# Kernel tuning notes

Hardware: AMD Instinct MI355X
Metric: run time of the kernel (lower is better)

Reference implementation:

```python
import jax, jax.numpy as jnp
import numpy as np
import math

D_MODEL = 128      # embedding_dim
D_STATE = 64
D_CONV = 4
NHEADS = 4         # d_inner / headdim (Mamba2 default headdim=64)
HEADDIM = 64
D_INNER = 256      # expand * d_model
CONV_DIM = 384     # d_inner + 2*ngroups*d_state (ngroups=1)
D_IN_PROJ = 644    # 2*d_inner + 2*ngroups*d_state + nheads
NLAYERS = 2
INPUT_DIM = 768
EPS = 1e-5


def setup_inputs() -> dict:
    key = jax.random.key(0)
    ks = jax.random.split(key, 20)
    rn = lambda k, s, sd=0.02: jax.random.normal(k, s, jnp.float32) * sd
    return {
        "x": jax.random.normal(ks[0], (16, 1024, INPUT_DIM), jnp.float32),
        "fc1_W": rn(ks[1], (INPUT_DIM, D_MODEL)),
        "fc1_b": jnp.zeros((D_MODEL,), jnp.float32),
        "ln_w": jnp.ones((NLAYERS, D_MODEL), jnp.float32),
        "ln_b": jnp.zeros((NLAYERS, D_MODEL), jnp.float32),
        "in_W": rn(ks[2], (NLAYERS, D_MODEL, D_IN_PROJ)),
        "conv_w": rn(ks[3], (NLAYERS, D_CONV, CONV_DIM), 0.1),
        "conv_b": jnp.zeros((NLAYERS, CONV_DIM), jnp.float32),
        "dt_bias": rn(ks[4], (NLAYERS, NHEADS), 0.5),
        "A_log": jnp.log(jax.random.uniform(ks[5], (NLAYERS, NHEADS), jnp.float32, 1.0, 16.0)),
        "Dp": jnp.ones((NLAYERS, NHEADS), jnp.float32),
        "rms_w": jnp.ones((NLAYERS, D_INNER), jnp.float32),
        "out_W": rn(ks[6], (NLAYERS, D_INNER, D_MODEL)),
        "fc2_W1": rn(ks[7], (D_MODEL, D_MODEL)),
        "fc2_b1": jnp.zeros((D_MODEL,), jnp.float32),
        "fc2_W2": rn(ks[8], (D_MODEL, 6)),
        "fc2_b2": jnp.zeros((6,), jnp.float32),
    }


def _pos_embedding(L):
    pos = jnp.arange(L, dtype=jnp.float32)[:, None]                       # (L,1)
    div = jnp.exp(jnp.arange(0, D_MODEL, 2, dtype=jnp.float32) * (-math.log(10000.0) / D_MODEL))
    pe = jnp.zeros((L, D_MODEL), jnp.float32)
    pe = pe.at[:, 0::2].set(jnp.sin(pos * div))
    pe = pe.at[:, 1::2].set(jnp.cos(pos * div))
    return pe[None]                                                        # (1,L,D)


def _layernorm(x, w, b):
    mu = jnp.mean(x, -1, keepdims=True)
    var = jnp.mean(jnp.square(x - mu), -1, keepdims=True)
    return (x - mu) * jax.lax.rsqrt(var + EPS) * w + b


def _mamba2(u, in_W, conv_w, conv_b, dt_bias, A_log, Dp, rms_w, out_W):
    b, l, _ = u.shape
    zxbcdt = u @ in_W                                                      # (b,l,644)
    z = zxbcdt[..., :D_INNER]
    xBC = zxbcdt[..., D_INNER:D_INNER + CONV_DIM]
    dt = jax.nn.softplus(zxbcdt[..., D_INNER + CONV_DIM:] + dt_bias)       # (b,l,h)
    # causal depthwise conv1d (width 4) + SiLU
    xp = jnp.pad(xBC, ((0, 0), (D_CONV - 1, 0), (0, 0)))
    xc = conv_b
    for k in range(D_CONV):
        xc = xc + conv_w[k] * xp[:, k:k + l, :]
    xc = jax.nn.silu(xc)                                                   # (b,l,384)
    xh = xc[..., :D_INNER].reshape(b, l, NHEADS, HEADDIM)                  # (b,l,h,p)
    B = xc[..., D_INNER:D_INNER + D_STATE]                                 # (b,l,n)
    C = xc[..., D_INNER + D_STATE:]                                        # (b,l,n)
    A = -jnp.exp(A_log)                                                    # (h,)
    dA = jnp.exp(dt * A)                                                   # (b,l,h)
    dtx = dt[..., None] * xh                                               # (b,l,h,p)

    def step(h, inp):
        dA_t, dtx_t, B_t, C_t = inp                                        # (b,h),(b,h,p),(b,n),(b,n)
        h = dA_t[..., None, None] * h + dtx_t[..., None] * B_t[:, None, None, :]
        y = jnp.einsum('bhpn,bn->bhp', h, C_t)
        return h, y

    h0 = jnp.zeros((b, NHEADS, HEADDIM, D_STATE), u.dtype)
    _, ys = jax.lax.scan(step, h0, (dA.transpose(1, 0, 2), dtx.transpose(1, 0, 2, 3),
                                    B.transpose(1, 0, 2), C.transpose(1, 0, 2)))
    y = ys.transpose(1, 0, 2, 3) + Dp[None, None, :, None] * xh            # (b,l,h,p)
    y = y.reshape(b, l, D_INNER)
    # gated RMSNorm: rmsnorm(y * silu(z)) * weight
    y = y * jax.nn.silu(z)
    y = y * jax.lax.rsqrt(jnp.mean(jnp.square(y), -1, keepdims=True) + EPS) * rms_w
    return y @ out_W


def reference(x, fc1_W, fc1_b, ln_w, ln_b, in_W, conv_w, conv_b, dt_bias,
              A_log, Dp, rms_w, out_W, fc2_W1, fc2_b1, fc2_W2, fc2_b2):
    h = x @ fc1_W + fc1_b                                                  # (b,l,128)
    h = h + _pos_embedding(h.shape[1])
    for i in range(NLAYERS):
        res = h
        hn = _layernorm(h, ln_w[i], ln_b[i])
        h = _mamba2(hn, in_W[i], conv_w[i], conv_b[i], dt_bias[i],
                    A_log[i], Dp[i], rms_w[i], out_W[i]) + res
        # dropout: identity in eval mode
    h = jax.nn.leaky_relu(h @ fc2_W1 + fc2_b1, negative_slope=0.1)
    return h @ fc2_W2 + fc2_b2                                             # (b,l,6)
```

## Files before the change

### kernel.cpp

```cpp
#include <hip/hip_runtime.h>
#include <hip/hip_bf16.h>

#define BATCH 16
#define SEQ 1024
#define NROWS (BATCH*SEQ)
#define IN_DIM 768
#define DM 128
#define DIP 644
#define DI 256
#define CDIM 384
#define DST 64
#define NH 4
#define HD 64
#define CHUNK 64
#define NCHUNK (SEQ/CHUNK)

#define WB_FC1   0
#define WB_IN    98304
#define WB_OUT   263168
#define WB_FC2   328704
#define WB_TOTAL 345088

typedef __attribute__((ext_vector_type(8))) short short8;
typedef __attribute__((ext_vector_type(4))) float float4v;

__device__ __forceinline__ short f2b(float f) {
    unsigned u = __builtin_bit_cast(unsigned, f);
    u += 0x7fffu + ((u >> 16) & 1u);
    return (short)(u >> 16);
}
__device__ __forceinline__ short8 pack8f(float4 a, float4 b) {
    short8 r;
    r[0] = f2b(a.x); r[1] = f2b(a.y); r[2] = f2b(a.z); r[3] = f2b(a.w);
    r[4] = f2b(b.x); r[5] = f2b(b.y); r[6] = f2b(b.z); r[7] = f2b(b.w);
    return r;
}

__global__ void prep_weights(const float* __restrict__ fc1_W, const float* __restrict__ in_W,
                             const float* __restrict__ out_W, const float* __restrict__ fc2_W1,
                             short* __restrict__ wb) {
    int idx = blockIdx.x * 256 + threadIdx.x;
    if (idx < 98304) {
        int n = idx / 768, k = idx % 768;
        wb[WB_FC1 + idx] = f2b(fc1_W[k * 128 + n]);
        return;
    }
    idx -= 98304;
    if (idx < 2 * 82432) {
        int l = idx / 82432, r = idx % 82432;
        int n = r / 128, k = r % 128;
        wb[WB_IN + idx] = f2b(in_W[(size_t)l * 82432 + k * 644 + n]);
        return;
    }
    idx -= 164864;
    if (idx < 2 * 32768) {
        int l = idx / 32768, r = idx % 32768;
        int n = r / 256, k = r % 256;
        wb[WB_OUT + idx] = f2b(out_W[(size_t)l * 32768 + k * 128 + n]);
        return;
    }
    idx -= 65536;
    if (idx < 16384) {
        int n = idx / 128, k = idx % 128;
        wb[WB_FC2 + idx] = f2b(fc2_W1[k * 128 + n]);
    }
}

#define GEMM_PROLOGUE() \
    int tid = threadIdx.x; \
    int lane = tid & 63; \
    int m = lane & 15; \
    int kq = (lane >> 4) * 8; \
    int w = tid >> 6; \
    int mrow = (w & 3) * 16; \
    int ngrp = w >> 2; \
    int a_off = (mrow + m) * 72 + kq; \
    int b_off = (ngrp * 64 + m) * 72 + kq; \
    int ar = tid >> 3; \
    int ak = (tid & 7) * 8; \
    (void)ar; (void)ak; \
    float4v acc[4]; \
    acc[0] = (float4v)0.f; acc[1] = (float4v)0.f; acc[2] = (float4v)0.f; acc[3] = (float4v)0.f;

#define GEMM_COMPUTE_TILE() \
    { \
        short8 a0 = *reinterpret_cast<const short8*>(&As[a_off]); \
        short8 a1 = *reinterpret_cast<const short8*>(&As[a_off + 32]); \
        _Pragma("unroll") \
        for (int nt = 0; nt < 4; nt++) { \
            short8 b0 = *reinterpret_cast<const short8*>(&Bt[b_off + nt * 16 * 72]); \
            short8 b1 = *reinterpret_cast<const short8*>(&Bt[b_off + nt * 16 * 72 + 32]); \
            acc[nt] = __builtin_amdgcn_mfma_f32_16x16x32_bf16(a0, b0, acc[nt], 0, 0, 0); \
            acc[nt] = __builtin_amdgcn_mfma_f32_16x16x32_bf16(a1, b1, acc[nt], 0, 0, 0); \
        } \
    }

#define GEMM_STAGE_B(wtptr, LDB, k0) \
    _Pragma("unroll") \
    for (int i = 0; i < 2; i++) { \
        int idx = tid + i * 512; \
        int n = idx >> 3, kk = (idx & 7) * 8; \
        *reinterpret_cast<short8*>(&Bt[n * 72 + kk]) = \
            *reinterpret_cast<const short8*>(&wtptr[n * (LDB) + (k0) + kk]); \
    }

__global__ __launch_bounds__(512) void fc1_mfma(const float* __restrict__ x,
                                                const short* __restrict__ wt,
                                                const float* __restrict__ bias,
                                                float* __restrict__ h) {
    __shared__ short As[64 * 72];
    __shared__ short Bt[128 * 72];
    GEMM_PROLOGUE();
    int row0 = blockIdx.x * 64;
    for (int kt = 0; kt < 12; kt++) {
        int k0 = kt * 64;
        if (kt) __syncthreads();
        {
            const float* src = x + (size_t)(row0 + ar) * IN_DIM + k0 + ak;
            float4 v0 = *(const float4*)src;
            float4 v1 = *(const float4*)(src + 4);
            *reinterpret_cast<short8*>(&As[ar * 72 + ak]) = pack8f(v0, v1);
        }
        GEMM_STAGE_B(wt, 768, k0);
        __syncthreads();
        GEMM_COMPUTE_TILE();
    }
    #pragma unroll
    for (int nt = 0; nt < 4; nt++) {
        int col = ngrp * 64 + nt * 16 + m;
        float bv = bias[col];
        float div = expf(-(float)(col & ~1) * 0.071955784f);
        #pragma unroll
        for (int r = 0; r < 4; r++) {
            int row = row0 + mrow + (lane >> 4) * 4 + r;
            int t = row & (SEQ - 1);
            float arg = (float)t * div;
            float pe = (col & 1) ? cosf(arg) : sinf(arg);
            h[(size_t)row * DM + col] = acc[nt][r] + bv + pe;
        }
    }
}

__global__ __launch_bounds__(512) void inproj_ln_mfma(const float* __restrict__ h,
                                                      const float* __restrict__ lnw,
                                                      const float* __restrict__ lnb,
                                                      const short* __restrict__ wb,
                                                      float* __restrict__ zx, int layer) {
    __shared__ short As[64 * 72];
    __shared__ short Bt[128 * 72];
    __shared__ float mu_s[64], rs_s[64];
    GEMM_PROLOGUE();
    int row0 = blockIdx.x * 64;
    int ncol0 = blockIdx.y * 128;
    const short* wt = wb + WB_IN + (size_t)layer * 82432;
    {
        int r = tid >> 3, j = tid & 7;
        const float4* hr = (const float4*)(h + (size_t)(row0 + r) * DM + j * 16);
        float s1 = 0.f, s2 = 0.f;
        #pragma unroll
        for (int i = 0; i < 4; i++) {
            float4 v = hr[i];
            s1 += v.x + v.y + v.z + v.w;
            s2 += v.x * v.x + v.y * v.y + v.z * v.z + v.w * v.w;
        }
        #pragma unroll
        for (int o = 1; o < 8; o <<= 1) { s1 += __shfl_xor(s1, o); s2 += __shfl_xor(s2, o); }
        if (j == 0) {
            float mu = s1 * (1.f / 128.f);
            mu_s[r] = mu;
            rs_s[r] = rsqrtf(s2 * (1.f / 128.f) - mu * mu + 1e-5f);
        }
    }
    __syncthreads();
    for (int kt = 0; kt < 2; kt++) {
        int k0 = kt * 64;
        if (kt) __syncthreads();
        {
            int k = k0 + ak;
            const float* src = h + (size_t)(row0 + ar) * DM + k;
            float4 v0 = *(const float4*)src;
            float4 v1 = *(const float4*)(src + 4);
            float4 w0 = *(const float4*)(lnw + layer * DM + k);
            float4 w1 = *(const float4*)(lnw + layer * DM + k + 4);
            float4 b0 = *(const float4*)(lnb + layer * DM + k);
            float4 b1 = *(const float4*)(lnb + layer * DM + k + 4);
            float mu = mu_s[ar], rs = rs_s[ar];
            v0.x = (v0.x - mu) * rs * w0.x + b0.x; v0.y = (v0.y - mu) * rs * w0.y + b0.y;
            v0.z = (v0.z - mu) * rs * w0.z + b0.z; v0.w = (v0.w - mu) * rs * w0.w + b0.w;
            v1.x = (v1.x - mu) * rs * w1.x + b1.x; v1.y = (v1.y - mu) * rs * w1.y + b1.y;
            v1.z = (v1.z - mu) * rs * w1.z + b1.z; v1.w = (v1.w - mu) * rs * w1.w + b1.w;
            *reinterpret_cast<short8*>(&As[ar * 72 + ak]) = pack8f(v0, v1);
        }
        #pragma unroll
        for (int i = 0; i < 2; i++) {
            int idx = tid + i * 512;
            int n = idx >> 3, kk = (idx & 7) * 8;
            int col = ncol0 + n;
            short8 bv = (short8)0;
            if (col < DIP) bv = *reinterpret_cast<const short8*>(&wt[col * 128 + k0 + kk]);
            *reinterpret_cast<short8*>(&Bt[n * 72 + kk]) = bv;
        }
        __syncthreads();
        GEMM_COMPUTE_TILE();
    }
    #pragma unroll
    for (int nt = 0; nt < 4; nt++) {
        int col = ncol0 + ngrp * 64 + nt * 16 + m;
        if (col < DIP) {
            #pragma unroll
            for (int r = 0; r < 4; r++) {
                int row = row0 + mrow + (lane >> 4) * 4 + r;
                zx[(size_t)row * DIP + col] = acc[nt][r];
            }
        }
    }
}

__global__ void conv_kernel(const float* __restrict__ zx, const float* __restrict__ convw,
                            const float* __restrict__ convb, const float* __restrict__ dt_bias,
                            float* __restrict__ xc, float* __restrict__ dtb, int layer) {
    int c = threadIdx.x;
    int row0 = blockIdx.x * 4;
    int l0 = row0 & (SEQ - 1);
    const float* cw = convw + (size_t)layer * 4 * CDIM;
    float w0 = cw[c], w1 = cw[CDIM + c], w2 = cw[2 * CDIM + c], w3 = cw[3 * CDIM + c];
    float bb = convb[layer * CDIM + c];
    float v[7];
    #pragma unroll
    for (int i = 0; i < 7; i++) {
        int rr = row0 + i - 3;
        v[i] = (l0 + i - 3 >= 0) ? zx[(size_t)rr * DIP + DI + c] : 0.f;
    }
    #pragma unroll
    for (int j = 0; j < 4; j++) {
        float acc = bb + w0 * v[j] + w1 * v[j + 1] + w2 * v[j + 2] + w3 * v[j + 3];
        float sv = acc / (1.f + expf(-acc));
        xc[(size_t)(row0 + j) * CDIM + c] = sv;
    }
    if (c < 16) {
        int j = c >> 2, hh = c & 3;
        int row = row0 + j;
        float raw = zx[(size_t)row * DIP + DI + CDIM + hh] + dt_bias[layer * NH + hh];
        float dt = (raw > 20.f) ? raw : log1pf(expf(raw));
        dtb[row * NH + hh] = dt;
    }
}

__global__ __launch_bounds__(256) void chunk_state_mfma(const float* __restrict__ xc,
                                                        const float* __restrict__ dtb,
                                                        const float* __restrict__ A_log,
                                                        float* __restrict__ Sloc,
                                                        float* __restrict__ decay, int layer) {
    __shared__ short XTw[64 * 72];
    __shared__ short BT[64 * 72];
    __shared__ float wst[64];
    int bid = blockIdx.x;
    int c  = bid & (NCHUNK - 1);
    int hh = (bid >> 4) & (NH - 1);
    int b  = bid >> 6;
    int tid = threadIdx.x;
    int row0 = b * SEQ + c * CHUNK;
    float A = -expf(A_log[layer * NH + hh]);

    if (tid < CHUNK) {
        float dtv = dtb[(row0 + tid) * NH + hh];
        float l = dtv * A;
        #pragma unroll
        for (int o = 1; o < 64; o <<= 1) { float v = __shfl_up(l, o); if (tid >= o) l += v; }
        float Ltot = __shfl(l, 63);
        wst[tid] = expf(Ltot - l) * dtv;
        if (tid == 63) decay[bid] = expf(Ltot);
    }
    __syncthreads();
    {
        int p = tid & 63;
        int tb0 = tid >> 6;
        #pragma unroll
        for (int i = 0; i < 2; i++) {
            int t0 = (tb0 + i * 4) * 8;
            short8 xv, bv;
            #pragma unroll
            for (int j = 0; j < 8; j++) {
                int t = t0 + j;
                const float* xr = xc + (size_t)(row0 + t) * CDIM;
                xv[j] = f2b(xr[hh * HD + p] * wst[t]);
                bv[j] = f2b(xr[DI + p]);
            }
            *reinterpret_cast<short8*>(&XTw[p * 72 + t0]) = xv;
            *reinterpret_cast<short8*>(&BT[p * 72 + t0]) = bv;
        }
    }
    __syncthreads();

    int lane = tid & 63;
    int m = lane & 15;
    int kq = (lane >> 4) * 8;
    int w = tid >> 6;
    int a_off = (w * 16 + m) * 72 + kq;
    float4v acc[4];
    acc[0] = (float4v)0.f; acc[1] = (float4v)0.f; acc[2] = (float4v)0.f; acc[3] = (float4v)0.f;
    short8 a0 = *reinterpret_cast<const short8*>(&XTw[a_off]);
    short8 a1 = *reinterpret_cast<const short8*>(&XTw[a_off + 32]);
    #pragma unroll
    for (int nt = 0; nt < 4; nt++) {
        int bo = (nt * 16 + m) * 72 + kq;
        short8 b0 = *reinterpret_cast<const short8*>(&BT[bo]);
        short8 b1 = *reinterpret_cast<const short8*>(&BT[bo + 32]);
        acc[nt] = __builtin_amdgcn_mfma_f32_16x16x32_bf16(a0, b0, acc[nt], 0, 0, 0);
        acc[nt] = __builtin_amdgcn_mfma_f32_16x16x32_bf16(a1, b1, acc[nt], 0, 0, 0);
    }
    float* Sp = Sloc + (size_t)bid * (HD * DST);
    int tq = (lane >> 4) * 4;
    #pragma unroll
    for (int nt = 0; nt < 4; nt++) {
        #pragma unroll
        for (int r = 0; r < 4; r++) {
            int p = w * 16 + tq + r;
            int n = nt * 16 + m;
            Sp[p * DST + n] = acc[nt][r];
        }
    }
}

__global__ void chunk_scan_kernel(const float* __restrict__ Sloc, const float* __restrict__ decay,
                                  float* __restrict__ hstart) {
    int bh = blockIdx.x;
    int tid = threadIdx.x;
    float hreg[16];
    #pragma unroll
    for (int k = 0; k < 16; k++) hreg[k] = 0.f;
    for (int c = 0; c < NCHUNK; c++) {
        size_t base = ((size_t)bh * NCHUNK + c) * (HD * DST);
        float d = decay[bh * NCHUNK + c];
        #pragma unroll
        for (int k = 0; k < 16; k++) {
            int i = tid + k * 256;
            hstart[base + i] = hreg[k];
            hreg[k] = d * hreg[k] + Sloc[base + i];
        }
    }
}

__global__ __launch_bounds__(256) void chunk_out_mfma(const float* __restrict__ xc,
                                                      const float* __restrict__ dtb,
                                                      const float* __restrict__ A_log,
                                                      const float* __restrict__ Dpw,
                                                      const float* __restrict__ hstart,
                                                      float* __restrict__ y, int layer) {
    __shared__ short Cb[64 * 72];
    __shared__ short Bb[64 * 72];
    __shared__ short XT[64 * 72];
    __shared__ short HT[64 * 72];
    __shared__ float Ls[64], dts[64];
    int bid = blockIdx.x;
    int c  = bid & (NCHUNK - 1);
    int hh = (bid >> 4) & (NH - 1);
    int b  = bid >> 6;
    int tid = threadIdx.x;
    int row0 = b * SEQ + c * CHUNK;
    float A = -expf(A_log[layer * NH + hh]);
    float Dph = Dpw[layer * NH + hh];

    if (tid < CHUNK) {
        float dtv = dtb[(row0 + tid) * NH + hh];
        float l = dtv * A;
        #pragma unroll
        for (int o = 1; o < 64; o <<= 1) { float v = __shfl_up(l, o); if (tid >= o) l += v; }
        Ls[tid] = l;
        dts[tid] = dtv;
    }
    {
        int p = tid & 63;
        int tb0 = tid >> 6;
        #pragma unroll
        for (int i = 0; i < 2; i++) {
            int t0 = (tb0 + i * 4) * 8;
            short8 xv;
            #pragma unroll
            for (int j = 0; j < 8; j++) {
                const float* xr = xc + (size_t)(row0 + t0 + j) * CDIM;
                xv[j] = f2b(xr[hh * HD + p]);
            }
            *reinterpret_cast<short8*>(&XT[p * 72 + t0]) = xv;
        }
    }
    #pragma unroll
    for (int i = 0; i < 2; i++) {
        int idx = tid + i * 256;
        int t = idx >> 3, cb = (idx & 7) * 8;
        const float* xr = xc + (size_t)(row0 + t) * CDIM;
        float4 b0 = *(const float4*)(xr + DI + cb);
        float4 b1 = *(const float4*)(xr + DI + cb + 4);
        *reinterpret_cast<short8*>(&Bb[t * 72 + cb]) = pack8f(b0, b1);
        float4 c0 = *(const float4*)(xr + DI + DST + cb);
        float4 c1 = *(const float4*)(xr + DI + DST + cb + 4);
        *reinterpret_cast<short8*>(&Cb[t * 72 + cb]) = pack8f(c0, c1);
    }
    {
        const float* hs = hstart + (size_t)bid * (HD * DST);
        #pragma unroll
        for (int i = 0; i < 2; i++) {
            int idx = tid + i * 256;
            int pp = idx >> 3, nb = (idx & 7) * 8;
            float4 a0 = *(const float4*)(hs + pp * 64 + nb);
            float4 a1 = *(const float4*)(hs + pp * 64 + nb + 4);
            *reinterpret_cast<short8*>(&HT[pp * 72 + nb]) = pack8f(a0, a1);
        }
    }
    __syncthreads();

    int lane = tid & 63;
    int m = lane & 15;
    int kq = (lane >> 4) * 8;
    int w = tid >> 6;
    int tq = (lane >> 4) * 4;
    int a_off = (w * 16 + m) * 72 + kq;

    short8 ca0 = *reinterpret_cast<const short8*>(&Cb[a_off]);
    short8 ca1 = *reinterpret_cast<const short8*>(&Cb[a_off + 32]);

    float4v g[4], ir[4];
    #pragma unroll
    for (int i = 0; i < 4; i++) { g[i] = (float4v)0.f; ir[i] = (float4v)0.f; }
    #pragma unroll
    for (int st = 0; st < 4; st++) {
        int bo = (st * 16 + m) * 72 + kq;
        short8 b0 = *reinterpret_cast<const short8*>(&Bb[bo]);
        short8 b1 = *reinterpret_cast<const short8*>(&Bb[bo + 32]);
        g[st] = __builtin_amdgcn_mfma_f32_16x16x32_bf16(ca0, b0, g[st], 0, 0, 0);
        g[st] = __builtin_amdgcn_mfma_f32_16x16x32_bf16(ca1, b1, g[st], 0, 0, 0);
        short8 h0 = *reinterpret_cast<const short8*>(&HT[bo]);
        short8 h1 = *reinterpret_cast<const short8*>(&HT[bo + 32]);
        ir[st] = __builtin_amdgcn_mfma_f32_16x16x32_bf16(ca0, h0, ir[st], 0, 0, 0);
        ir[st] = __builtin_amdgcn_mfma_f32_16x16x32_bf16(ca1, h1, ir[st], 0, 0, 0);
    }
    __syncthreads();
    #pragma unroll
    for (int st = 0; st < 4; st++) {
        #pragma unroll
        for (int r = 0; r < 4; r++) {
            int t = w * 16 + tq + r;
            int s = st * 16 + m;
            float mv = 0.f;
            if (s <= t) mv = g[st][r] * expf(Ls[t] - Ls[s]) * dts[s];
            Bb[t * 72 + s] = f2b(mv);
        }
    }
    __syncthreads();
    float4v yi[4];
    #pragma unroll
    for (int i = 0; i < 4; i++) yi[i] = (float4v)0.f;
    short8 ma0 = *reinterpret_cast<const short8*>(&Bb[a_off]);
    short8 ma1 = *reinterpret_cast<const short8*>(&Bb[a_off + 32]);
    #pragma unroll
    for (int pt = 0; pt < 4; pt++) {
        int bo = (pt * 16 + m) * 72 + kq;
        short8 x0 = *reinterpret_cast<const short8*>(&XT[bo]);
        short8 x1 = *reinterpret_cast<const short8*>(&XT[bo + 32]);
        yi[pt] = __builtin_amdgcn_mfma_f32_16x16x32_bf16(ma0, x0, yi[pt], 0, 0, 0);
        yi[pt] = __builtin_amdgcn_mfma_f32_16x16x32_bf16(ma1, x1, yi[pt], 0, 0, 0);
    }
    #pragma unroll
    for (int r = 0; r < 4; r++) {
        int t = w * 16 + tq + r;
        float et = expf(Ls[t]);
        const float* xr = xc + (size_t)(row0 + t) * CDIM + hh * HD;
        float* yr = y + (size_t)(row0 + t) * DI + hh * HD;
        #pragma unroll
        for (int pt = 0; pt < 4; pt++) {
            int p = pt * 16 + m;
            yr[p] = yi[pt][r] + et * ir[pt][r] + Dph * xr[p];
        }
    }
}

__global__ __launch_bounds__(512) void outproj_gate_mfma(const float* __restrict__ yb,
                                                         const float* __restrict__ zx,
                                                         const float* __restrict__ rmsw,
                                                         const short* __restrict__ wb,
                                                         float* __restrict__ h, int layer) {
    __shared__ short As[64 * 72];
    __shared__ short Bt[128 * 72];
    __shared__ float rs_s[64];
    GEMM_PROLOGUE();
    int row0 = blockIdx.x * 64;
    const short* wt = wb + WB_OUT + (size_t)layer * 32768;
    {
        int r = tid >> 3, j = tid & 7;
        const float4* yr = (const float4*)(yb + (size_t)(row0 + r) * DI + j * 32);
        const float4* zr = (const float4*)(zx + (size_t)(row0 + r) * DIP + j * 32);
        float s2 = 0.f;
        #pragma unroll
        for (int i = 0; i < 8; i++) {
            float4 yv = yr[i], zv = zr[i];
            float v;
            v = yv.x * (zv.x / (1.f + expf(-zv.x))); s2 += v * v;
            v = yv.y * (zv.y / (1.f + expf(-zv.y))); s2 += v * v;
            v = yv.z * (zv.z / (1.f + expf(-zv.z))); s2 += v * v;
            v = yv.w * (zv.w / (1.f + expf(-zv.w))); s2 += v * v;
        }
        #pragma unroll
        for (int o = 1; o < 8; o <<= 1) s2 += __shfl_xor(s2, o);
        if (j == 0) rs_s[r] = rsqrtf(s2 * (1.f / 256.f) + 1e-5f);
    }
    __syncthreads();
    for (int kt = 0; kt < 4; kt++) {
        int k0 = kt * 64;
        if (kt) __syncthreads();
        {
            int k = k0 + ak;
            const float* ysrc = yb + (size_t)(row0 + ar) * DI + k;
            const float* zsrc = zx + (size_t)(row0 + ar) * DIP + k;
            float4 y0 = *(const float4*)ysrc;
            float4 y1 = *(const float4*)(ysrc + 4);
            float4 z0 = *(const float4*)zsrc;
            float4 z1 = *(const float4*)(zsrc + 4);
            float4 w0 = *(const float4*)(rmsw + layer * DI + k);
            float4 w1 = *(const float4*)(rmsw + layer * DI + k + 4);
            float rs = rs_s[ar];
            y0.x = y0.x * (z0.x / (1.f + expf(-z0.x))) * rs * w0.x;
            y0.y = y0.y * (z0.y / (1.f + expf(-z0.y))) * rs * w0.y;
            y0.z = y0.z * (z0.z / (1.f + expf(-z0.z))) * rs * w0.z;
            y0.w = y0.w * (z0.w / (1.f + expf(-z0.w))) * rs * w0.w;
            y1.x = y1.x * (z1.x / (1.f + expf(-z1.x))) * rs * w1.x;
            y1.y = y1.y * (z1.y / (1.f + expf(-z1.y))) * rs * w1.y;
            y1.z = y1.z * (z1.z / (1.f + expf(-z1.z))) * rs * w1.z;
            y1.w = y1.w * (z1.w / (1.f + expf(-z1.w))) * rs * w1.w;
            *reinterpret_cast<short8*>(&As[ar * 72 + ak]) = pack8f(y0, y1);
        }
        GEMM_STAGE_B(wt, 256, k0);
        __syncthreads();
        GEMM_COMPUTE_TILE();
    }
    #pragma unroll
    for (int nt = 0; nt < 4; nt++) {
        int col = ngrp * 64 + nt * 16 + m;
        #pragma unroll
        for (int r = 0; r < 4; r++) {
            int row = row0 + mrow + (lane >> 4) * 4 + r;
            size_t i = (size_t)row * DM + col;
            h[i] = h[i] + acc[nt][r];
        }
    }
}

__global__ __launch_bounds__(512) void fc2ab_mfma(const float* __restrict__ h,
                                                  const short* __restrict__ wb,
                                                  const float* __restrict__ b1,
                                                  const float* __restrict__ W2,
                                                  const float* __restrict__ b2,
                                                  float* __restrict__ out) {
    __shared__ short As[64 * 72];
    __shared__ short Bt[128 * 72];
    __shared__ float h2s[64][132];
    __shared__ float w2s[768];
    GEMM_PROLOGUE();
    int row0 = blockIdx.x * 64;
    const short* wt = wb + WB_FC2;
    for (int i = tid; i < 768; i += 512) w2s[i] = W2[i];
    for (int kt = 0; kt < 2; kt++) {
        int k0 = kt * 64;
        if (kt) __syncthreads();
        {
            const float* src = h + (size_t)(row0 + ar) * DM + k0 + ak;
            float4 v0 = *(const float4*)src;
            float4 v1 = *(const float4*)(src + 4);
            *reinterpret_cast<short8*>(&As[ar * 72 + ak]) = pack8f(v0, v1);
        }
        GEMM_STAGE_B(wt, 128, k0);
        __syncthreads();
        GEMM_COMPUTE_TILE();
    }
    #pragma unroll
    for (int nt = 0; nt < 4; nt++) {
        int col = ngrp * 64 + nt * 16 + m;
        float bv = b1[col];
        #pragma unroll
        for (int r = 0; r < 4; r++) {
            int rr = mrow + (lane >> 4) * 4 + r;
            float o = acc[nt][r] + bv;
            h2s[rr][col] = (o > 0.f) ? o : 0.1f * o;
        }
    }
    __syncthreads();
    if (tid < 384) {
        int r = tid / 6, cc = tid % 6;
        float acc2 = b2[cc];
        #pragma unroll 16
        for (int k = 0; k < 128; k++) acc2 += h2s[r][k] * w2s[k * 6 + cc];
        out[(size_t)(row0 + r) * 6 + cc] = acc2;
    }
}

extern "C" void kernel_launch(void* const* d_in, const int* in_sizes, int n_in,
                              void* d_out, int out_size, void* d_ws, size_t ws_size,
                              hipStream_t stream) {
    const float* x       = (const float*)d_in[0];
    const float* fc1_W   = (const float*)d_in[1];
    const float* fc1_b   = (const float*)d_in[2];
    const float* ln_w    = (const float*)d_in[3];
    const float* ln_b    = (const float*)d_in[4];
    const float* in_W    = (const float*)d_in[5];
    const float* conv_w  = (const float*)d_in[6];
    const float* conv_b  = (const float*)d_in[7];
    const float* dt_bias = (const float*)d_in[8];
    const float* A_log   = (const float*)d_in[9];
    const float* Dp      = (const float*)d_in[10];
    const float* rms_w   = (const float*)d_in[11];
    const float* out_W   = (const float*)d_in[12];
    const float* fc2_W1  = (const float*)d_in[13];
    const float* fc2_b1  = (const float*)d_in[14];
    const float* fc2_W2  = (const float*)d_in[15];
    const float* fc2_b2  = (const float*)d_in[16];
    float* out = (float*)d_out;

    float* ws = (float*)d_ws;
    float* h     = ws;
    float* zx    = h     + (size_t)NROWS * DM;
    float* xc    = zx    + (size_t)NROWS * DIP;
    float* dtb   = xc    + (size_t)NROWS * CDIM;
    float* yb    = dtb   + (size_t)NROWS * NH;
    float* Sloc  = yb    + (size_t)NROWS * DI;
    float* hstr  = Sloc  + (size_t)BATCH*NH*NCHUNK*HD*DST;
    float* decay = hstr  + (size_t)BATCH*NH*NCHUNK*HD*DST;
    short* wb    = (short*)(decay + 1024);

    prep_weights<<<1348, 256, 0, stream>>>(fc1_W, in_W, out_W, fc2_W1, wb);
    fc1_mfma<<<NROWS / 64, 512, 0, stream>>>(x, wb + WB_FC1, fc1_b, h);

    for (int layer = 0; layer < 2; layer++) {
        inproj_ln_mfma<<<dim3(NROWS / 64, 6), 512, 0, stream>>>(h, ln_w, ln_b, wb, zx, layer);
        conv_kernel<<<NROWS / 4, CDIM, 0, stream>>>(zx, conv_w, conv_b, dt_bias, xc, dtb, layer);
        chunk_state_mfma<<<BATCH*NH*NCHUNK, 256, 0, stream>>>(xc, dtb, A_log, Sloc, decay, layer);
        chunk_scan_kernel<<<BATCH*NH, 256, 0, stream>>>(Sloc, decay, hstr);
        chunk_out_mfma<<<BATCH*NH*NCHUNK, 256, 0, stream>>>(xc, dtb, A_log, Dp, hstr, yb, layer);
        outproj_gate_mfma<<<NROWS / 64, 512, 0, stream>>>(yb, zx, rms_w, wb, h, layer);
    }

    fc2ab_mfma<<<NROWS / 64, 512, 0, stream>>>(h, wb, fc2_b1, fc2_W2, fc2_b2, out);
}
```

Measured before the change: 301.3 us.

## Store Mamba2 intermediates in bf16 and split in-proj output into separate buffers

Intermediate activations between kernels (conv input and output, chunk states, chunk start states, y) are now stored as bf16 instead of fp32. The in-proj output is split into a z buffer, a bf16 xBC buffer and a dt buffer. This roughly halves global memory traffic across the layer pipeline, which is memory-bound, and removes fp32-to-bf16 packing in consumers. The cost is an extra rounding of the scan states and outputs. The chunk scan now uses vectorized contiguous per-thread access.

```diff
diff --git a/kernel.cpp b/kernel.cpp
--- a/kernel.cpp
+++ b/kernel.cpp
@@ -28,6 +28,10 @@
     unsigned u = __builtin_bit_cast(unsigned, f);
     u += 0x7fffu + ((u >> 16) & 1u);
     return (short)(u >> 16);
+}
+__device__ __forceinline__ float s2f(short s) {
+    unsigned u = ((unsigned)(unsigned short)s) << 16;
+    return __builtin_bit_cast(float, u);
 }
 __device__ __forceinline__ short8 pack8f(float4 a, float4 b) {
     short8 r;
@@ -145,7 +149,9 @@
                                                       const float* __restrict__ lnw,
                                                       const float* __restrict__ lnb,
                                                       const short* __restrict__ wb,
-                                                      float* __restrict__ zx, int layer) {
+                                                      float* __restrict__ zbuf,
+                                                      short* __restrict__ xbc,
+                                                      float* __restrict__ dtraw, int layer) {
     __shared__ short As[64 * 72];
     __shared__ short Bt[128 * 72];
     __shared__ float mu_s[64], rs_s[64];
@@ -206,19 +212,32 @@
     #pragma unroll
     for (int nt = 0; nt < 4; nt++) {
         int col = ncol0 + ngrp * 64 + nt * 16 + m;
-        if (col < DIP) {
+        if (col < DI) {
             #pragma unroll
             for (int r = 0; r < 4; r++) {
                 int row = row0 + mrow + (lane >> 4) * 4 + r;
-                zx[(size_t)row * DIP + col] = acc[nt][r];
+                zbuf[(size_t)row * DI + col] = acc[nt][r];
             }
-        }
-    }
-}
-
-__global__ void conv_kernel(const float* __restrict__ zx, const float* __restrict__ convw,
-                            const float* __restrict__ convb, const float* __restrict__ dt_bias,
-                            float* __restrict__ xc, float* __restrict__ dtb, int layer) {
+        } else if (col < DI + CDIM) {
+            #pragma unroll
+            for (int r = 0; r < 4; r++) {
+                int row = row0 + mrow + (lane >> 4) * 4 + r;
+                xbc[(size_t)row * CDIM + (col - DI)] = f2b(acc[nt][r]);
+            }
+        } else if (col < DIP) {
+            #pragma unroll
+            for (int r = 0; r < 4; r++) {
+                int row = row0 + mrow + (lane >> 4) * 4 + r;
+                dtraw[(size_t)row * NH + (col - DI - CDIM)] = acc[nt][r];
+            }
+        }
+    }
+}
+
+__global__ void conv_kernel(const short* __restrict__ xbc, const float* __restrict__ dtraw,
+                            const float* __restrict__ convw, const float* __restrict__ convb,
+                            const float* __restrict__ dt_bias,
+                            short* __restrict__ xcb, float* __restrict__ dtb, int layer) {
     int c = threadIdx.x;
     int row0 = blockIdx.x * 4;
     int l0 = row0 & (SEQ - 1);
@@ -229,27 +248,27 @@
     #pragma unroll
     for (int i = 0; i < 7; i++) {
         int rr = row0 + i - 3;
-        v[i] = (l0 + i - 3 >= 0) ? zx[(size_t)rr * DIP + DI + c] : 0.f;
+        v[i] = (l0 + i - 3 >= 0) ? s2f(xbc[(size_t)rr * CDIM + c]) : 0.f;
     }
     #pragma unroll
     for (int j = 0; j < 4; j++) {
         float acc = bb + w0 * v[j] + w1 * v[j + 1] + w2 * v[j + 2] + w3 * v[j + 3];
         float sv = acc / (1.f + expf(-acc));
-        xc[(size_t)(row0 + j) * CDIM + c] = sv;
+        xcb[(size_t)(row0 + j) * CDIM + c] = f2b(sv);
     }
     if (c < 16) {
         int j = c >> 2, hh = c & 3;
         int row = row0 + j;
-        float raw = zx[(size_t)row * DIP + DI + CDIM + hh] + dt_bias[layer * NH + hh];
+        float raw = dtraw[(size_t)row * NH + hh] + dt_bias[layer * NH + hh];
         float dt = (raw > 20.f) ? raw : log1pf(expf(raw));
         dtb[row * NH + hh] = dt;
     }
 }
 
-__global__ __launch_bounds__(256) void chunk_state_mfma(const float* __restrict__ xc,
+__global__ __launch_bounds__(256) void chunk_state_mfma(const short* __restrict__ xcb,
                                                         const float* __restrict__ dtb,
                                                         const float* __restrict__ A_log,
-                                                        float* __restrict__ Sloc,
+                                                        short* __restrict__ Slocb,
                                                         float* __restrict__ decay, int layer) {
     __shared__ short XTw[64 * 72];
     __shared__ short BT[64 * 72];
@@ -282,9 +301,9 @@
             #pragma unroll
             for (int j = 0; j < 8; j++) {
                 int t = t0 + j;
-                const float* xr = xc + (size_t)(row0 + t) * CDIM;
-                xv[j] = f2b(xr[hh * HD + p] * wst[t]);
-                bv[j] = f2b(xr[DI + p]);
+                const short* xr = xcb + (size_t)(row0 + t) * CDIM;
+                xv[j] = f2b(s2f(xr[hh * HD + p]) * wst[t]);
+                bv[j] = xr[DI + p];
             }
             *reinterpret_cast<short8*>(&XTw[p * 72 + t0]) = xv;
             *reinterpret_cast<short8*>(&BT[p * 72 + t0]) = bv;
@@ -309,7 +328,7 @@
         acc[nt] = __builtin_amdgcn_mfma_f32_16x16x32_bf16(a0, b0, acc[nt], 0, 0, 0);
         acc[nt] = __builtin_amdgcn_mfma_f32_16x16x32_bf16(a1, b1, acc[nt], 0, 0, 0);
     }
-    float* Sp = Sloc + (size_t)bid * (HD * DST);
+    short* Sp = Slocb + (size_t)bid * (HD * DST);
     int tq = (lane >> 4) * 4;
     #pragma unroll
     for (int nt = 0; nt < 4; nt++) {
@@ -317,36 +336,42 @@
         for (int r = 0; r < 4; r++) {
             int p = w * 16 + tq + r;
             int n = nt * 16 + m;
-            Sp[p * DST + n] = acc[nt][r];
-        }
-    }
-}
-
-__global__ void chunk_scan_kernel(const float* __restrict__ Sloc, const float* __restrict__ decay,
-                                  float* __restrict__ hstart) {
+            Sp[p * DST + n] = f2b(acc[nt][r]);
+        }
+    }
+}
+
+__global__ void chunk_scan_kernel(const short* __restrict__ Slocb, const float* __restrict__ decay,
+                                  short* __restrict__ hstrb) {
     int bh = blockIdx.x;
     int tid = threadIdx.x;
     float hreg[16];
     #pragma unroll
     for (int k = 0; k < 16; k++) hreg[k] = 0.f;
     for (int c = 0; c < NCHUNK; c++) {
-        size_t base = ((size_t)bh * NCHUNK + c) * (HD * DST);
+        size_t base = ((size_t)bh * NCHUNK + c) * (HD * DST) + tid * 16;
         float d = decay[bh * NCHUNK + c];
-        #pragma unroll
-        for (int k = 0; k < 16; k++) {
-            int i = tid + k * 256;
-            hstart[base + i] = hreg[k];
-            hreg[k] = d * hreg[k] + Sloc[base + i];
-        }
-    }
-}
-
-__global__ __launch_bounds__(256) void chunk_out_mfma(const float* __restrict__ xc,
+        short8 s0 = *reinterpret_cast<const short8*>(&Slocb[base]);
+        short8 s1 = *reinterpret_cast<const short8*>(&Slocb[base + 8]);
+        short8 h0, h1;
+        #pragma unroll
+        for (int k = 0; k < 8; k++) { h0[k] = f2b(hreg[k]); h1[k] = f2b(hreg[8 + k]); }
+        *reinterpret_cast<short8*>(&hstrb[base]) = h0;
+        *reinterpret_cast<short8*>(&hstrb[base + 8]) = h1;
+        #pragma unroll
+        for (int k = 0; k < 8; k++) {
+            hreg[k]     = d * hreg[k]     + s2f(s0[k]);
+            hreg[8 + k] = d * hreg[8 + k] + s2f(s1[k]);
+        }
+    }
+}
+
+__global__ __launch_bounds__(256) void chunk_out_mfma(const short* __restrict__ xcb,
                                                       const float* __restrict__ dtb,
                                                       const float* __restrict__ A_log,
                                                       const float* __restrict__ Dpw,
-                                                      const float* __restrict__ hstart,
-                                                      float* __restrict__ y, int layer) {
+                                                      const short* __restrict__ hstrb,
+                                                      short* __restrict__ ybb, int layer) {
     __shared__ short Cb[64 * 72];
     __shared__ short Bb[64 * 72];
     __shared__ short XT[64 * 72];
@@ -377,10 +402,8 @@
             int t0 = (tb0 + i * 4) * 8;
             short8 xv;
             #pragma unroll
-            for (int j = 0; j < 8; j++) {
-                const float* xr = xc + (size_t)(row0 + t0 + j) * CDIM;
-                xv[j] = f2b(xr[hh * HD + p]);
-            }
+            for (int j = 0; j < 8; j++)
+                xv[j] = xcb[(size_t)(row0 + t0 + j) * CDIM + hh * HD + p];
             *reinterpret_cast<short8*>(&XT[p * 72 + t0]) = xv;
         }
     }
@@ -388,23 +411,20 @@
     for (int i = 0; i < 2; i++) {
         int idx = tid + i * 256;
         int t = idx >> 3, cb = (idx & 7) * 8;
-        const float* xr = xc + (size_t)(row0 + t) * CDIM;
-        float4 b0 = *(const float4*)(xr + DI + cb);
-        float4 b1 = *(const float4*)(xr + DI + cb + 4);
-        *reinterpret_cast<short8*>(&Bb[t * 72 + cb]) = pack8f(b0, b1);
-        float4 c0 = *(const float4*)(xr + DI + DST + cb);
-        float4 c1 = *(const float4*)(xr + DI + DST + cb + 4);
-        *reinterpret_cast<short8*>(&Cb[t * 72 + cb]) = pack8f(c0, c1);
+        const short* xr = xcb + (size_t)(row0 + t) * CDIM;
+        *reinterpret_cast<short8*>(&Bb[t * 72 + cb]) =
+            *reinterpret_cast<const short8*>(&xr[DI + cb]);
+        *reinterpret_cast<short8*>(&Cb[t * 72 + cb]) =
+            *reinterpret_cast<const short8*>(&xr[DI + DST + cb]);
     }
     {
-        const float* hs = hstart + (size_t)bid * (HD * DST);
+        const short* hs = hstrb + (size_t)bid * (HD * DST);
         #pragma unroll
         for (int i = 0; i < 2; i++) {
             int idx = tid + i * 256;
             int pp = idx >> 3, nb = (idx & 7) * 8;
-            float4 a0 = *(const float4*)(hs + pp * 64 + nb);
-            float4 a1 = *(const float4*)(hs + pp * 64 + nb + 4);
-            *reinterpret_cast<short8*>(&HT[pp * 72 + nb]) = pack8f(a0, a1);
+            *reinterpret_cast<short8*>(&HT[pp * 72 + nb]) =
+                *reinterpret_cast<const short8*>(&hs[pp * 64 + nb]);
         }
     }
     __syncthreads();
@@ -464,18 +484,18 @@
     for (int r = 0; r < 4; r++) {
         int t = w * 16 + tq + r;
         float et = expf(Ls[t]);
-        const float* xr = xc + (size_t)(row0 + t) * CDIM + hh * HD;
-        float* yr = y + (size_t)(row0 + t) * DI + hh * HD;
+        const short* xr = xcb + (size_t)(row0 + t) * CDIM + hh * HD;
+        short* yr = ybb + (size_t)(row0 + t) * DI + hh * HD;
         #pragma unroll
         for (int pt = 0; pt < 4; pt++) {
             int p = pt * 16 + m;
-            yr[p] = yi[pt][r] + et * ir[pt][r] + Dph * xr[p];
-        }
-    }
-}
-
-__global__ __launch_bounds__(512) void outproj_gate_mfma(const float* __restrict__ yb,
-                                                         const float* __restrict__ zx,
+            yr[p] = f2b(yi[pt][r] + et * ir[pt][r] + Dph * s2f(xr[p]));
+        }
+    }
+}
+
+__global__ __launch_bounds__(512) void outproj_gate_mfma(const short* __restrict__ ybb,
+                                                         const float* __restrict__ zbuf,
                                                          const float* __restrict__ rmsw,
                                                          const short* __restrict__ wb,
                                                          float* __restrict__ h, int layer) {
@@ -487,17 +507,21 @@
     const short* wt = wb + WB_OUT + (size_t)layer * 32768;
     {
         int r = tid >> 3, j = tid & 7;
-        const float4* yr = (const float4*)(yb + (size_t)(row0 + r) * DI + j * 32);
-        const float4* zr = (const float4*)(zx + (size_t)(row0 + r) * DIP + j * 32);
+        const short8* yr = (const short8*)(ybb + (size_t)(row0 + r) * DI + j * 32);
+        const float4* zr = (const float4*)(zbuf + (size_t)(row0 + r) * DI + j * 32);
         float s2 = 0.f;
         #pragma unroll
-        for (int i = 0; i < 8; i++) {
-            float4 yv = yr[i], zv = zr[i];
-            float v;
-            v = yv.x * (zv.x / (1.f + expf(-zv.x))); s2 += v * v;
-            v = yv.y * (zv.y / (1.f + expf(-zv.y))); s2 += v * v;
-            v = yv.z * (zv.z / (1.f + expf(-zv.z))); s2 += v * v;
-            v = yv.w * (zv.w / (1.f + expf(-zv.w))); s2 += v * v;
+        for (int i = 0; i < 4; i++) {
+            short8 yv = yr[i];
+            #pragma unroll
+            for (int q = 0; q < 2; q++) {
+                float4 zv = zr[i * 2 + q];
+                float v;
+                v = s2f(yv[q*4+0]) * (zv.x / (1.f + expf(-zv.x))); s2 += v * v;
+                v = s2f(yv[q*4+1]) * (zv.y / (1.f + expf(-zv.y))); s2 += v * v;
+                v = s2f(yv[q*4+2]) * (zv.z / (1.f + expf(-zv.z))); s2 += v * v;
+                v = s2f(yv[q*4+3]) * (zv.w / (1.f + expf(-zv.w))); s2 += v * v;
+            }
         }
         #pragma unroll
         for (int o = 1; o < 8; o <<= 1) s2 += __shfl_xor(s2, o);
@@ -509,24 +533,23 @@
         if (kt) __syncthreads();
         {
             int k = k0 + ak;
-            const float* ysrc = yb + (size_t)(row0 + ar) * DI + k;
-            const float* zsrc = zx + (size_t)(row0 + ar) * DIP + k;
-            float4 y0 = *(const float4*)ysrc;
-            float4 y1 = *(const float4*)(ysrc + 4);
+            short8 yv = *(const short8*)(ybb + (size_t)(row0 + ar) * DI + k);
+            const float* zsrc = zbuf + (size_t)(row0 + ar) * DI + k;
             float4 z0 = *(const float4*)zsrc;
             float4 z1 = *(const float4*)(zsrc + 4);
             float4 w0 = *(const float4*)(rmsw + layer * DI + k);
             float4 w1 = *(const float4*)(rmsw + layer * DI + k + 4);
             float rs = rs_s[ar];
-            y0.x = y0.x * (z0.x / (1.f + expf(-z0.x))) * rs * w0.x;
-            y0.y = y0.y * (z0.y / (1.f + expf(-z0.y))) * rs * w0.y;
-            y0.z = y0.z * (z0.z / (1.f + expf(-z0.z))) * rs * w0.z;
-            y0.w = y0.w * (z0.w / (1.f + expf(-z0.w))) * rs * w0.w;
-            y1.x = y1.x * (z1.x / (1.f + expf(-z1.x))) * rs * w1.x;
-            y1.y = y1.y * (z1.y / (1.f + expf(-z1.y))) * rs * w1.y;
-            y1.z = y1.z * (z1.z / (1.f + expf(-z1.z))) * rs * w1.z;
-            y1.w = y1.w * (z1.w / (1.f + expf(-z1.w))) * rs * w1.w;
-            *reinterpret_cast<short8*>(&As[ar * 72 + ak]) = pack8f(y0, y1);
+            short8 av;
+            av[0] = f2b(s2f(yv[0]) * (z0.x / (1.f + expf(-z0.x))) * rs * w0.x);
+            av[1] = f2b(s2f(yv[1]) * (z0.y / (1.f + expf(-z0.y))) * rs * w0.y);
+            av[2] = f2b(s2f(yv[2]) * (z0.z / (1.f + expf(-z0.z))) * rs * w0.z);
+            av[3] = f2b(s2f(yv[3]) * (z0.w / (1.f + expf(-z0.w))) * rs * w0.w);
+            av[4] = f2b(s2f(yv[4]) * (z1.x / (1.f + expf(-z1.x))) * rs * w1.x);
+            av[5] = f2b(s2f(yv[5]) * (z1.y / (1.f + expf(-z1.y))) * rs * w1.y);
+            av[6] = f2b(s2f(yv[6]) * (z1.z / (1.f + expf(-z1.z))) * rs * w1.z);
+            av[7] = f2b(s2f(yv[7]) * (z1.w / (1.f + expf(-z1.w))) * rs * w1.w);
+            *reinterpret_cast<short8*>(&As[ar * 72 + ak]) = av;
         }
         GEMM_STAGE_B(wt, 256, k0);
         __syncthreads();
@@ -616,25 +639,30 @@
 
     float* ws = (float*)d_ws;
     float* h     = ws;
-    float* zx    = h     + (size_t)NROWS * DM;
-    float* xc    = zx    + (size_t)NROWS * DIP;
-    float* dtb   = xc    + (size_t)NROWS * CDIM;
-    float* yb    = dtb   + (size_t)NROWS * NH;
-    float* Sloc  = yb    + (size_t)NROWS * DI;
-    float* hstr  = Sloc  + (size_t)BATCH*NH*NCHUNK*HD*DST;
-    float* decay = hstr  + (size_t)BATCH*NH*NCHUNK*HD*DST;
-    short* wb    = (short*)(decay + 1024);
+    float* zbuf  = h     + (size_t)NROWS * DM;
+    float* dtraw = zbuf  + (size_t)NROWS * DI;
+    float* dtb   = dtraw + (size_t)NROWS * NH;
+    float* decay = dtb   + (size_t)NROWS * NH;
+    short* sbase = (short*)(decay + 1024);
+    short* xbc   = sbase;
+    short* xcb   = xbc   + (size_t)NROWS * CDIM;
+    short* ybb   = xcb   + (size_t)NROWS * CDIM;
+    short* Slocb = ybb   + (size_t)NROWS * DI;
+    short* hstrb = Slocb + (size_t)BATCH*NH*NCHUNK*HD*DST;
+    short* wb    = hstrb + (size_t)BATCH*NH*NCHUNK*HD*DST;
 
     prep_weights<<<1348, 256, 0, stream>>>(fc1_W, in_W, out_W, fc2_W1, wb);
     fc1_mfma<<<NROWS / 64, 512, 0, stream>>>(x, wb + WB_FC1, fc1_b, h);
 
     for (int layer = 0; layer < 2; layer++) {
-        inproj_ln_mfma<<<dim3(NROWS / 64, 6), 512, 0, stream>>>(h, ln_w, ln_b, wb, zx, layer);
-        conv_kernel<<<NROWS / 4, CDIM, 0, stream>>>(zx, conv_w, conv_b, dt_bias, xc, dtb, layer);
-        chunk_state_mfma<<<BATCH*NH*NCHUNK, 256, 0, stream>>>(xc, dtb, A_log, Sloc, decay, layer);
-        chunk_scan_kernel<<<BATCH*NH, 256, 0, stream>>>(Sloc, decay, hstr);
-        chunk_out_mfma<<<BATCH*NH*NCHUNK, 256, 0, stream>>>(xc, dtb, A_log, Dp, hstr, yb, layer);
-        outproj_gate_mfma<<<NROWS / 64, 512, 0, stream>>>(yb, zx, rms_w, wb, h, layer);
+        inproj_ln_mfma<<<dim3(NROWS / 64, 6), 512, 0, stream>>>(h, ln_w, ln_b, wb,
+                                                                zbuf, xbc, dtraw, layer);
+        conv_kernel<<<NROWS / 4, CDIM, 0, stream>>>(xbc, dtraw, conv_w, conv_b, dt_bias,
+                                                    xcb, dtb, layer);
+        chunk_state_mfma<<<BATCH*NH*NCHUNK, 256, 0, stream>>>(xcb, dtb, A_log, Slocb, decay, layer);
+        chunk_scan_kernel<<<BATCH*NH, 256, 0, stream>>>(Slocb, decay, hstrb);
+        chunk_out_mfma<<<BATCH*NH*NCHUNK, 256, 0, stream>>>(xcb, dtb, A_log, Dp, hstrb, ybb, layer);
+        outproj_gate_mfma<<<NROWS / 64, 512, 0, stream>>>(ybb, zbuf, rms_w, wb, h, layer);
     }
 
     fc2ab_mfma<<<NROWS / 64, 512, 0, stream>>>(h, wb, fc2_b1, fc2_W2, fc2_b2, out);
```

Result: faster. 274.8 us (-8.8%).
